# Optimization experiments

Hardware: AMD Instinct MI355X
Metric: run time of the kernel (lower is better)

## Reference

```python
import jax, jax.numpy as jnp
import numpy as np

B, S, E, H = 8, 2048, 1024, 64

def setup_inputs() -> dict:
    key = jax.random.key(0)
    ks = jax.random.split(key, 7)
    scale = 1.0 / np.sqrt(E)
    return {
        "x": jax.random.normal(ks[0], (B, S, E), dtype=jnp.float32),
        "mask": jnp.ones((B, S), dtype=jnp.int32),
        "Wq": jax.random.uniform(ks[1], (E, H), jnp.float32, -scale, scale),
        "bq": jax.random.uniform(ks[2], (H,), jnp.float32, -scale, scale),
        "Wk": jax.random.uniform(ks[3], (E, H), jnp.float32, -scale, scale),
        "bk": jax.random.uniform(ks[4], (H,), jnp.float32, -scale, scale),
        "Wv": jax.random.uniform(ks[5], (E, H), jnp.float32, -scale, scale),
        "bv": jax.random.uniform(ks[6], (H,), jnp.float32, -scale, scale),
    }

def reference(x, mask, Wq, bq, Wk, bk, Wv, bv):
    # q,k,v: [B,S,H]
    q = jnp.einsum('bse,eh->bsh', x, Wq) + bq
    k = jnp.einsum('bse,eh->bsh', x, Wk) + bk
    v = jnp.einsum('bse,eh->bsh', x, Wv) + bv
    # scores: [B,S,S]
    scores = jnp.einsum('bqh,bkh->bqk', q, k) / jnp.sqrt(jnp.asarray(H, q.dtype))
    causal = jnp.tril(jnp.ones((S, S), dtype=bool))  # [S,S]
    pad = (mask != 0)[:, None, :]                    # [B,1,S]
    neg_inf = jnp.asarray(float('-inf'), scores.dtype)
    scores = jnp.where(causal[None] & pad, scores, neg_inf)
    attn = jax.nn.softmax(scores, axis=-1)
    return jnp.einsum('bqk,bkh->bqh', attn, v)
```

## Files before the change

### kernel.cpp

```cpp
#include <hip/hip_runtime.h>
#include <hip/hip_bf16.h>

#define S_ 2048
#define E_ 1024
#define QNC 16

typedef __attribute__((ext_vector_type(8))) short short8;
typedef __attribute__((ext_vector_type(4))) float f32x4;

__device__ __forceinline__ short f2bf(float f) {
    __hip_bfloat16 h = __float2bfloat16(f);
    return *(short*)&h;
}

__device__ __forceinline__ void g2l16(const void* g, void* l) {
    __builtin_amdgcn_global_load_lds(
        (const __attribute__((address_space(1))) void*)g,
        (__attribute__((address_space(3))) void*)l, 16, 0, 0);
}

__global__ __launch_bounds__(256) void prep_weights(
    const float* __restrict__ Wq, const float* __restrict__ Wk,
    const float* __restrict__ Wv, unsigned short* __restrict__ Wtt)
{
    int tw = blockIdx.x * 256 + threadIdx.x;
    int nt = tw >> 11;
    int lane = tw & 63;
    int n = nt * 16 + (lane & 15);
    int h = n & 63;
    const float* W = (n < 64) ? Wq : (n < 128) ? Wk : Wv;
    int k0 = ((tw >> 6) & 31) * 32 + (lane >> 4) * 8;
    short8 o;
    #pragma unroll
    for (int e = 0; e < 8; ++e) o[e] = f2bf(W[(k0 + e) * 64 + h]);
    *(short8*)(Wtt + (size_t)tw * 8) = o;
}

__global__ __launch_bounds__(256, 4) void qkv_main(
    const float* __restrict__ x, const unsigned short* __restrict__ Wtt,
    const float* __restrict__ bq, const float* __restrict__ bk,
    const float* __restrict__ bv,
    unsigned short* __restrict__ Q, unsigned short* __restrict__ K,
    unsigned short* __restrict__ Vt)
{
    __shared__ __align__(16) char lds[5][8192];
    int tid = threadIdx.x;
    int wave = tid >> 6, lane = tid & 63;
    int lo = lane & 15, hi = lane >> 4;
    int wn = wave;
    int rowbase = blockIdx.x * 32;
    const char* xg = (const char*)x;

    f32x4 acc[2][3];
    #pragma unroll
    for (int a = 0; a < 2; ++a)
        #pragma unroll
        for (int j = 0; j < 3; ++j) acc[a][j] = (f32x4){0.f, 0.f, 0.f, 0.f};

    #define STAGE(bb, kc)                                                         \
        {                                                                         \
            _Pragma("unroll")                                                     \
            for (int i = 0; i < 2; ++i) {                                         \
                int u_lin = i * 256 + tid;                                        \
                int r = u_lin >> 4, u = u_lin & 15;                               \
                const char* src = xg + (size_t)(rowbase + r) * 4096 + (kc) * 256  \
                                  + (((u & 8) | ((u & 7) ^ (r & 7))) << 4);       \
                g2l16(src, &lds[bb][(i * 256 + wave * 64) * 16]);                 \
            }                                                                     \
        }

    #define LOADB(dst, t)                                                         \
        {                                                                         \
            _Pragma("unroll")                                                     \
            for (int j = 0; j < 3; ++j)                                           \
                _Pragma("unroll")                                                 \
                for (int kk = 0; kk < 2; ++kk)                                    \
                    dst[j][kk] = *(const short8*)(Wtt +                           \
                        (size_t)(((wn * 3 + j) * 32 + (t) * 2 + kk) * 64 + lane) * 8); \
        }

    #define COMPUTE(bfr, t)                                                       \
        {                                                                         \
            const char* lx = lds[(t) % 5];                                        \
            _Pragma("unroll")                                                     \
            for (int rt = 0; rt < 2; ++rt) {                                      \
                int r = rt * 16 + lo;                                             \
                _Pragma("unroll")                                                 \
                for (int kk = 0; kk < 2; ++kk) {                                  \
                    int u0 = kk * 8 + hi * 2;                                     \
                    float4 a0 = *(const float4*)(lx + r * 256                     \
                        + (((u0 & 8) | ((u0 & 7) ^ (lo & 7))) << 4));             \
                    float4 a1 = *(const float4*)(lx + r * 256                     \
                        + ((((u0 + 1) & 8) | (((u0 + 1) & 7) ^ (lo & 7))) << 4)); \
                    short8 af;                                                    \
                    af[0] = f2bf(a0.x); af[1] = f2bf(a0.y);                       \
                    af[2] = f2bf(a0.z); af[3] = f2bf(a0.w);                       \
                    af[4] = f2bf(a1.x); af[5] = f2bf(a1.y);                       \
                    af[6] = f2bf(a1.z); af[7] = f2bf(a1.w);                       \
                    _Pragma("unroll")                                             \
                    for (int j = 0; j < 3; ++j)                                   \
                        acc[rt][j] = __builtin_amdgcn_mfma_f32_16x16x32_bf16(     \
                            af, bfr[j][kk], acc[rt][j], 0, 0, 0);                 \
                }                                                                 \
            }                                                                     \
        }

    #define WAITQ(t)                                                              \
        {                                                                         \
            if ((t) <= 11)      asm volatile("s_waitcnt vmcnt(12)" ::: "memory"); \
            else if ((t) == 12) asm volatile("s_waitcnt vmcnt(10)" ::: "memory"); \
            else if ((t) == 13) asm volatile("s_waitcnt vmcnt(8)" ::: "memory");  \
            else                asm volatile("s_waitcnt vmcnt(6)" ::: "memory");  \
        }

    short8 bfrA[3][2], bfrB[3][2];

    LOADB(bfrA, 0);
    __builtin_amdgcn_sched_barrier(0);
    STAGE(0, 0); STAGE(1, 1); STAGE(2, 2); STAGE(3, 3);
    __builtin_amdgcn_sched_barrier(0);
    asm volatile("s_waitcnt vmcnt(6)" ::: "memory");
    __builtin_amdgcn_sched_barrier(0);
    __builtin_amdgcn_s_barrier();

    for (int tb = 0; tb < 8; ++tb) {
        int t0 = 2 * tb, t1 = 2 * tb + 1;
        LOADB(bfrB, t1);
        COMPUTE(bfrA, t0);
        if (t0 + 4 < QNC) STAGE((t0 + 4) % 5, t0 + 4);
        __builtin_amdgcn_sched_barrier(0);
        WAITQ(t0);
        __builtin_amdgcn_sched_barrier(0);
        __builtin_amdgcn_s_barrier();
        if (t1 + 1 < QNC) LOADB(bfrA, t1 + 1);
        COMPUTE(bfrB, t1);
        if (t1 + 4 < QNC) STAGE((t1 + 4) % 5, t1 + 4);
        if (t1 < QNC - 1) {
            __builtin_amdgcn_sched_barrier(0);
            WAITQ(t1);
            __builtin_amdgcn_sched_barrier(0);
            __builtin_amdgcn_s_barrier();
        }
    }
    #undef STAGE
    #undef LOADB
    #undef COMPUTE
    #undef WAITQ

    #pragma unroll
    for (int rt = 0; rt < 2; ++rt) {
        #pragma unroll
        for (int j = 0; j < 3; ++j) {
            int n = wn * 48 + j * 16 + lo;
            #pragma unroll
            for (int r = 0; r < 4; ++r) {
                int row = rowbase + rt * 16 + 4 * hi + r;
                float v = acc[rt][j][r];
                if (n < 64) {
                    Q[(size_t)row * 64 + n] = (unsigned short)f2bf(v + bq[n]);
                } else if (n < 128) {
                    int h = n - 64;
                    K[(size_t)row * 64 + h] = (unsigned short)f2bf(v + bk[h]);
                } else {
                    int h = n - 128;
                    int b = row >> 11, s = row & (S_ - 1);
                    Vt[((size_t)b * 64 + h) * S_ + s] = (unsigned short)f2bf(v + bv[h]);
                }
            }
        }
    }
}

__global__ __launch_bounds__(256) void attn_stage(
    const unsigned short* __restrict__ Q, const unsigned short* __restrict__ K,
    const unsigned short* __restrict__ Vt, const int* __restrict__ mask,
    float* __restrict__ part)
{
    __shared__ __align__(16) char kv[3][16384];
    __shared__ __align__(16) unsigned short p_lds[4][16][72];
    int tid = threadIdx.x;
    int wave = tid >> 6, lane = tid & 63;
    int lo = lane & 15, hi = lane >> 4;
    int blk = blockIdx.x;
    int c = blk & 3;
    int pr = blk >> 2;
    int b = pr & 7;
    int qt64 = 31 - (pr >> 3);
    int nkt = qt64 + 1;
    int chunk = (nkt + 3) >> 2;
    int kt0 = c * chunk;
    int kt1 = min(kt0 + chunk, nkt);
    int ntile = kt1 - kt0;
    int qrow0 = qt64 * 64 + wave * 16;

    f32x4 o[4];
    float ps[4] = {0.f, 0.f, 0.f, 0.f};
    #pragma unroll
    for (int i = 0; i < 4; ++i) o[i] = (f32x4){0.f, 0.f, 0.f, 0.f};

    #define ASTAGE(bb, kt)                                                        \
        {                                                                         \
            int kbase_ = (kt) * 64;                                               \
            const char* kg = (const char*)K + (size_t)(b * S_ + kbase_) * 128;    \
            const char* vg = (const char*)Vt + (size_t)b * 64 * 4096 + kbase_ * 2;\
            _Pragma("unroll")                                                     \
            for (int j = 0; j < 2; ++j) {                                         \
                int r = (j * 4 + wave) * 8 + (lane >> 3);                         \
                int un = lane & 7;                                                \
                g2l16(kg + r * 128 + ((un ^ (r & 7)) << 4),                       \
                      &kv[bb][(j * 4 + wave) * 1024]);                            \
                g2l16(vg + (size_t)r * 4096 + ((un ^ (r & 7)) << 4),              \
                      &kv[bb][8192 + (j * 4 + wave) * 1024]);                     \
            }                                                                     \
        }

    if (ntile > 0) {
        const unsigned short* qp = Q + ((size_t)(b * S_ + qrow0 + lo)) * 64 + 8 * hi;
        short8 qf0 = *(const short8*)(qp);
        short8 qf1 = *(const short8*)(qp + 32);

        unsigned mbits = 0;
        for (int tt = 0; tt < 8; ++tt) {
            if (tt < ntile) {
                int kbase = (kt0 + tt) * 64;
                #pragma unroll
                for (int nt = 0; nt < 4; ++nt)
                    if (mask[b * S_ + kbase + nt * 16 + lo] != 0)
                        mbits |= (1u << (tt * 4 + nt));
            }
        }
        asm volatile("s_waitcnt vmcnt(0)" ::: "memory");
        __builtin_amdgcn_sched_barrier(0);

        ASTAGE(0, kt0);
        if (ntile > 1) ASTAGE(1, kt0 + 1);
        __builtin_amdgcn_sched_barrier(0);
        if (ntile > 1) asm volatile("s_waitcnt vmcnt(4)" ::: "memory");
        else           asm volatile("s_waitcnt vmcnt(0)" ::: "memory");
        __builtin_amdgcn_sched_barrier(0);
        __builtin_amdgcn_s_barrier();

        for (int t = 0; t < ntile; ++t) {
            int kbase = (kt0 + t) * 64;
            const char* kb = kv[t % 3];
            const char* vb = kv[t % 3] + 8192;

            f32x4 s[4];
            #pragma unroll
            for (int i = 0; i < 4; ++i) s[i] = (f32x4){0.f, 0.f, 0.f, 0.f};
            #pragma unroll
            for (int nt = 0; nt < 4; ++nt) {
                short8 kf0 = *(const short8*)(kb + (nt * 16 + lo) * 128 + ((hi ^ (lo & 7)) << 4));
                short8 kf1 = *(const short8*)(kb + (nt * 16 + lo) * 128 + (((4 + hi) ^ (lo & 7)) << 4));
                s[nt] = __builtin_amdgcn_mfma_f32_16x16x32_bf16(qf0, kf0, s[nt], 0, 0, 0);
                s[nt] = __builtin_amdgcn_mfma_f32_16x16x32_bf16(qf1, kf1, s[nt], 0, 0, 0);
            }

            #pragma unroll
            for (int nt = 0; nt < 4; ++nt) {
                int kpos = kbase + nt * 16 + lo;
                bool mok = (mbits >> (t * 4 + nt)) & 1;
                #pragma unroll
                for (int r = 0; r < 4; ++r) {
                    int qpos = qrow0 + 4 * hi + r;
                    bool ok = mok && (kpos <= qpos);
                    float pv = ok ? __expf(s[nt][r] * 0.125f) : 0.f;
                    ps[r] += pv;
                    p_lds[wave][4 * hi + r][nt * 16 + lo] = (unsigned short)f2bf(pv);
                }
            }

            #pragma unroll
            for (int kk = 0; kk < 2; ++kk) {
                short8 pf = *(const short8*)&p_lds[wave][lo][kk * 32 + 8 * hi];
                #pragma unroll
                for (int nt = 0; nt < 4; ++nt) {
                    short8 vf = *(const short8*)(vb + (nt * 16 + lo) * 128
                                                 + (((kk * 4 + hi) ^ (lo & 7)) << 4));
                    o[nt] = __builtin_amdgcn_mfma_f32_16x16x32_bf16(pf, vf, o[nt], 0, 0, 0);
                }
            }

            if (t + 2 < ntile) ASTAGE((t + 2) % 3, kt0 + t + 2);
            __builtin_amdgcn_sched_barrier(0);
            if (t + 1 < ntile) {
                if (t + 2 < ntile) asm volatile("s_waitcnt vmcnt(4)" ::: "memory");
                else               asm volatile("s_waitcnt vmcnt(0)" ::: "memory");
                __builtin_amdgcn_sched_barrier(0);
                __builtin_amdgcn_s_barrier();
            }
        }
    }
    #undef ASTAGE

    float l[4];
    #pragma unroll
    for (int r = 0; r < 4; ++r) {
        float v = ps[r];
        v += __shfl_xor(v, 1);
        v += __shfl_xor(v, 2);
        v += __shfl_xor(v, 4);
        v += __shfl_xor(v, 8);
        l[r] = v;
    }

    int tile16 = b * 128 + qt64 * 4 + wave;
    float* pp = part + (((size_t)c * 1024 + tile16) * 64 + lane) * 20;
    #pragma unroll
    for (int nt = 0; nt < 4; ++nt) *(f32x4*)(pp + nt * 4) = o[nt];
    f32x4 ll;
    #pragma unroll
    for (int r = 0; r < 4; ++r) ll[r] = l[r];
    *(f32x4*)(pp + 16) = ll;
}

__global__ __launch_bounds__(256) void attn_comb(
    const float* __restrict__ part, float* __restrict__ out)
{
    int g = blockIdx.x * 256 + threadIdx.x;
    int tile = g >> 6, lane = g & 63;
    int lo = lane & 15, hi = lane >> 4;
    int b = tile >> 7, qt = tile & 127;
    int qrow0 = qt * 16;

    f32x4 o[4];
    float l[4] = {0.f, 0.f, 0.f, 0.f};
    #pragma unroll
    for (int i = 0; i < 4; ++i) o[i] = (f32x4){0.f, 0.f, 0.f, 0.f};

    #pragma unroll
    for (int c = 0; c < 4; ++c) {
        const float* pp = part + (((size_t)c * 1024 + tile) * 64 + lane) * 20;
        #pragma unroll
        for (int nt = 0; nt < 4; ++nt) {
            f32x4 po = *(const f32x4*)(pp + nt * 4);
            #pragma unroll
            for (int r = 0; r < 4; ++r) o[nt][r] += po[r];
        }
        f32x4 pl = *(const f32x4*)(pp + 16);
        #pragma unroll
        for (int r = 0; r < 4; ++r) l[r] += pl[r];
    }

    #pragma unroll
    for (int nt = 0; nt < 4; ++nt) {
        #pragma unroll
        for (int r = 0; r < 4; ++r) {
            int qpos = qrow0 + 4 * hi + r;
            out[((size_t)(b * S_ + qpos)) * 64 + nt * 16 + lo] =
                (l[r] > 0.f) ? o[nt][r] / l[r] : 0.f;
        }
    }
}

extern "C" void kernel_launch(void* const* d_in, const int* in_sizes, int n_in,
                              void* d_out, int out_size, void* d_ws, size_t ws_size,
                              hipStream_t stream) {
    const float* x   = (const float*)d_in[0];
    const int*   msk = (const int*)d_in[1];
    const float* Wq  = (const float*)d_in[2];
    const float* bq  = (const float*)d_in[3];
    const float* Wk  = (const float*)d_in[4];
    const float* bk  = (const float*)d_in[5];
    const float* Wv  = (const float*)d_in[6];
    const float* bv  = (const float*)d_in[7];
    float* outp = (float*)d_out;

    char* w = (char*)d_ws;
    unsigned short* Wtt = (unsigned short*)w;
    unsigned short* Qb = (unsigned short*)(w + 0x080000);
    unsigned short* Kb = (unsigned short*)(w + 0x280000);
    unsigned short* Vt = (unsigned short*)(w + 0x480000);
    float* partp = (float*)(w + 0x680000);

    prep_weights<<<dim3(96), dim3(256), 0, stream>>>(Wq, Wk, Wv, Wtt);
    qkv_main<<<dim3(512), dim3(256), 0, stream>>>(x, Wtt, bq, bk, bv, Qb, Kb, Vt);
    attn_stage<<<dim3(1024), dim3(256), 0, stream>>>(Qb, Kb, Vt, msk, partp);
    attn_comb<<<dim3(256), dim3(256), 0, stream>>>(partp, outp);
}
```

Before: 56.56 us.

## Halve the QKV row tile and stage the epilogue through LDS

```diff
diff --git a/kernel.cpp b/kernel.cpp
--- a/kernel.cpp
+++ b/kernel.cpp
@@ -43,30 +43,26 @@
     unsigned short* __restrict__ Q, unsigned short* __restrict__ K,
     unsigned short* __restrict__ Vt)
 {
-    __shared__ __align__(16) char lds[5][8192];
+    __shared__ __align__(16) char lds[5][4096];
+    __shared__ __align__(16) char eq[16 * 272];
+    __shared__ __align__(16) unsigned short ev[64 * 18];
     int tid = threadIdx.x;
     int wave = tid >> 6, lane = tid & 63;
     int lo = lane & 15, hi = lane >> 4;
     int wn = wave;
-    int rowbase = blockIdx.x * 32;
+    int rowbase = blockIdx.x * 16;
     const char* xg = (const char*)x;
 
-    f32x4 acc[2][3];
-    #pragma unroll
-    for (int a = 0; a < 2; ++a)
-        #pragma unroll
-        for (int j = 0; j < 3; ++j) acc[a][j] = (f32x4){0.f, 0.f, 0.f, 0.f};
+    f32x4 acc[3];
+    #pragma unroll
+    for (int j = 0; j < 3; ++j) acc[j] = (f32x4){0.f, 0.f, 0.f, 0.f};
 
     #define STAGE(bb, kc)                                                         \
         {                                                                         \
-            _Pragma("unroll")                                                     \
-            for (int i = 0; i < 2; ++i) {                                         \
-                int u_lin = i * 256 + tid;                                        \
-                int r = u_lin >> 4, u = u_lin & 15;                               \
-                const char* src = xg + (size_t)(rowbase + r) * 4096 + (kc) * 256  \
-                                  + (((u & 8) | ((u & 7) ^ (r & 7))) << 4);       \
-                g2l16(src, &lds[bb][(i * 256 + wave * 64) * 16]);                 \
-            }                                                                     \
+            int r_ = tid >> 4, u_ = tid & 15;                                     \
+            const char* src = xg + (size_t)(rowbase + r_) * 4096 + (kc) * 256     \
+                              + (((u_ & 8) | ((u_ & 7) ^ (r_ & 7))) << 4);        \
+            g2l16(src, &lds[bb][wave * 1024]);                                    \
         }
 
     #define LOADB(dst, t)                                                         \
@@ -83,34 +79,29 @@
         {                                                                         \
             const char* lx = lds[(t) % 5];                                        \
             _Pragma("unroll")                                                     \
-            for (int rt = 0; rt < 2; ++rt) {                                      \
-                int r = rt * 16 + lo;                                             \
+            for (int kk = 0; kk < 2; ++kk) {                                      \
+                int u0 = kk * 8 + hi * 2;                                         \
+                float4 a0 = *(const float4*)(lx + lo * 256                        \
+                    + (((u0 & 8) | ((u0 & 7) ^ (lo & 7))) << 4));                 \
+                float4 a1 = *(const float4*)(lx + lo * 256                        \
+                    + ((((u0 + 1) & 8) | (((u0 + 1) & 7) ^ (lo & 7))) << 4));     \
+                short8 af;                                                        \
+                af[0] = f2bf(a0.x); af[1] = f2bf(a0.y);                           \
+                af[2] = f2bf(a0.z); af[3] = f2bf(a0.w);                           \
+                af[4] = f2bf(a1.x); af[5] = f2bf(a1.y);                           \
+                af[6] = f2bf(a1.z); af[7] = f2bf(a1.w);                           \
                 _Pragma("unroll")                                                 \
-                for (int kk = 0; kk < 2; ++kk) {                                  \
-                    int u0 = kk * 8 + hi * 2;                                     \
-                    float4 a0 = *(const float4*)(lx + r * 256                     \
-                        + (((u0 & 8) | ((u0 & 7) ^ (lo & 7))) << 4));             \
-                    float4 a1 = *(const float4*)(lx + r * 256                     \
-                        + ((((u0 + 1) & 8) | (((u0 + 1) & 7) ^ (lo & 7))) << 4)); \
-                    short8 af;                                                    \
-                    af[0] = f2bf(a0.x); af[1] = f2bf(a0.y);                       \
-                    af[2] = f2bf(a0.z); af[3] = f2bf(a0.w);                       \
-                    af[4] = f2bf(a1.x); af[5] = f2bf(a1.y);                       \
-                    af[6] = f2bf(a1.z); af[7] = f2bf(a1.w);                       \
-                    _Pragma("unroll")                                             \
-                    for (int j = 0; j < 3; ++j)                                   \
-                        acc[rt][j] = __builtin_amdgcn_mfma_f32_16x16x32_bf16(     \
-                            af, bfr[j][kk], acc[rt][j], 0, 0, 0);                 \
-                }                                                                 \
+                for (int j = 0; j < 3; ++j)                                       \
+                    acc[j] = __builtin_amdgcn_mfma_f32_16x16x32_bf16(             \
+                        af, bfr[j][kk], acc[j], 0, 0, 0);                         \
             }                                                                     \
         }
 
     #define WAITQ(t)                                                              \
         {                                                                         \
-            if ((t) <= 11)      asm volatile("s_waitcnt vmcnt(12)" ::: "memory"); \
-            else if ((t) == 12) asm volatile("s_waitcnt vmcnt(10)" ::: "memory"); \
-            else if ((t) == 13) asm volatile("s_waitcnt vmcnt(8)" ::: "memory");  \
-            else                asm volatile("s_waitcnt vmcnt(6)" ::: "memory");  \
+            if ((t) <= 11)      asm volatile("s_waitcnt vmcnt(8)" ::: "memory");  \
+            else if ((t) <= 13) asm volatile("s_waitcnt vmcnt(6)" ::: "memory");  \
+            else                asm volatile("s_waitcnt vmcnt(0)" ::: "memory");  \
         }
 
     short8 bfrA[3][2], bfrB[3][2];
@@ -119,7 +110,7 @@
     __builtin_amdgcn_sched_barrier(0);
     STAGE(0, 0); STAGE(1, 1); STAGE(2, 2); STAGE(3, 3);
     __builtin_amdgcn_sched_barrier(0);
-    asm volatile("s_waitcnt vmcnt(6)" ::: "memory");
+    asm volatile("s_waitcnt vmcnt(3)" ::: "memory");
     __builtin_amdgcn_sched_barrier(0);
     __builtin_amdgcn_s_barrier();
 
@@ -132,6 +123,7 @@
         WAITQ(t0);
         __builtin_amdgcn_sched_barrier(0);
         __builtin_amdgcn_s_barrier();
+
         if (t1 + 1 < QNC) LOADB(bfrA, t1 + 1);
         COMPUTE(bfrB, t1);
         if (t1 + 4 < QNC) STAGE((t1 + 4) % 5, t1 + 4);
@@ -147,27 +139,40 @@
     #undef COMPUTE
     #undef WAITQ
 
-    #pragma unroll
-    for (int rt = 0; rt < 2; ++rt) {
+    __syncthreads();
+    #pragma unroll
+    for (int j = 0; j < 3; ++j) {
+        int n = wn * 48 + j * 16 + lo;
         #pragma unroll
-        for (int j = 0; j < 3; ++j) {
-            int n = wn * 48 + j * 16 + lo;
-            #pragma unroll
-            for (int r = 0; r < 4; ++r) {
-                int row = rowbase + rt * 16 + 4 * hi + r;
-                float v = acc[rt][j][r];
-                if (n < 64) {
-                    Q[(size_t)row * 64 + n] = (unsigned short)f2bf(v + bq[n]);
-                } else if (n < 128) {
-                    int h = n - 64;
-                    K[(size_t)row * 64 + h] = (unsigned short)f2bf(v + bk[h]);
-                } else {
-                    int h = n - 128;
-                    int b = row >> 11, s = row & (S_ - 1);
-                    Vt[((size_t)b * 64 + h) * S_ + s] = (unsigned short)f2bf(v + bv[h]);
-                }
-            }
-        }
+        for (int r = 0; r < 4; ++r) {
+            int rr = 4 * hi + r;
+            float v = acc[j][r];
+            if (n < 64) {
+                *(unsigned short*)(eq + rr * 272 + n * 2) =
+                    (unsigned short)f2bf(v + bq[n]);
+            } else if (n < 128) {
+                *(unsigned short*)(eq + rr * 272 + n * 2) =
+                    (unsigned short)f2bf(v + bk[n - 64]);
+            } else {
+                ev[(n - 128) * 18 + rr] = (unsigned short)f2bf(v + bv[n - 128]);
+            }
+        }
+    }
+    __syncthreads();
+
+    {
+        int row = tid >> 4, seg = tid & 15;
+        short8 val = *(const short8*)(eq + row * 272 + seg * 16);
+        if (seg < 8)
+            *(short8*)(Q + (size_t)(rowbase + row) * 64 + seg * 8) = val;
+        else
+            *(short8*)(K + (size_t)(rowbase + row) * 64 + (seg - 8) * 8) = val;
+    }
+    if (tid < 128) {
+        int h = tid >> 1, su = tid & 1;
+        int b = rowbase >> 11, sl0 = rowbase & (S_ - 1);
+        short8 val = *(const short8*)((const char*)ev + h * 36 + su * 16);
+        *(short8*)(Vt + ((size_t)(b * 64 + h)) * S_ + sl0 + su * 8) = val;
     }
 }
 
@@ -374,7 +379,7 @@
     float* partp = (float*)(w + 0x680000);
 
     prep_weights<<<dim3(96), dim3(256), 0, stream>>>(Wq, Wk, Wv, Wtt);
-    qkv_main<<<dim3(512), dim3(256), 0, stream>>>(x, Wtt, bq, bk, bv, Qb, Kb, Vt);
+    qkv_main<<<dim3(1024), dim3(256), 0, stream>>>(x, Wtt, bq, bk, bv, Qb, Kb, Vt);
     attn_stage<<<dim3(1024), dim3(256), 0, stream>>>(Qb, Kb, Vt, msk, partp);
     attn_comb<<<dim3(256), dim3(256), 0, stream>>>(partp, outp);
 }
```

Result: slower. 61.14 us (+8.1%).
